# Kernel tuning notes

Hardware: AMD Instinct MI355X
Metric: run time of the kernel (lower is better)

The kernel has to match this reference:

```python
import jax, jax.numpy as jnp
import numpy as np

N, E, FEAT, HID, C, K = 100000, 1600000, 128, 256, 64, 10
AVG_DEG = 16.0

def prelu(x, a):
    return jnp.where(x >= 0, x, a * x)

def setup_inputs() -> dict:
    key = jax.random.key(0)
    ks = jax.random.split(key, 12)
    s = 0.05
    x = jax.random.normal(ks[0], (N, FEAT), jnp.float32)
    edge_index = jax.random.randint(ks[1], (2, E), 0, N, dtype=jnp.int32)
    # GCN-style symmetric norm magnitude ~ 1/deg so K-hop sums stay bounded
    norm = jax.random.uniform(ks[2], (E,), jnp.float32) * (1.0 / AVG_DEG)
    W1 = jax.random.normal(ks[3], (FEAT, HID), jnp.float32) * s
    b1 = jnp.zeros((HID,), jnp.float32)
    W2 = jax.random.normal(ks[4], (HID, HID), jnp.float32) * s
    b2 = jnp.zeros((HID,), jnp.float32)
    W3 = jax.random.normal(ks[5], (HID, HID), jnp.float32) * s
    b3 = jnp.zeros((HID,), jnp.float32)
    W4 = jax.random.normal(ks[6], (HID, C), jnp.float32) * s
    b4 = jnp.zeros((C,), jnp.float32)
    prelu_a = jnp.array(0.25, jnp.float32)
    proj_w = jax.random.normal(ks[7], (C, 1), jnp.float32) * s
    proj_b = jnp.zeros((1,), jnp.float32)
    return {"x": x, "edge_index": edge_index, "norm": norm,
            "W1": W1, "b1": b1, "W2": W2, "b2": b2, "W3": W3, "b3": b3,
            "W4": W4, "b4": b4, "prelu_a": prelu_a,
            "proj_w": proj_w, "proj_b": proj_b}

def reference(x, edge_index, norm, W1, b1, W2, b2, W3, b3, W4, b4, prelu_a, proj_w, proj_b):
    h = prelu(x @ W1 + b1, prelu_a)                      # [N, HID]
    h = prelu((h @ W2 + b2) + h, prelu_a)                # residual Dense
    h = prelu((h @ W3 + b3) + h, prelu_a)                # residual Dense
    z = h @ W4 + b4                                      # [N, C]
    # --- Prop: K hops of norm-weighted scatter-add over edge_index
    src, dst = edge_index[0], edge_index[1]
    def hop(h_cur, _):
        msg = norm[:, None] * h_cur[src]                 # [E, C] gather
        h_nxt = jax.ops.segment_sum(msg, dst, num_segments=N)
        return h_nxt, h_nxt
    _, hs = jax.lax.scan(hop, z, None, length=K)         # [K, N, C]
    pps = jnp.concatenate([z[None], hs], axis=0)         # [K+1, N, C]
    # adaptive per-hop retain score (DAGNN-style)
    score = jax.nn.sigmoid(jnp.einsum('knc,co->kn', pps, proj_w) + proj_b[0])  # [K+1, N]
    out = jnp.einsum('kn,knc->nc', score, pps)           # [N, C]
    return jax.nn.log_softmax(out, axis=1)
```

## Files before the change

kernel.cpp:

```cpp
#include <hip/hip_runtime.h>
#include <stdint.h>
#include <stddef.h>

#define FEATDIM 128
#define HIDDIM  256
#define CDIM    64
#define NHOPS   10

typedef __attribute__((ext_vector_type(8))) short bf16x8;
typedef __attribute__((ext_vector_type(4))) float f32x4;
typedef unsigned short u16;

__device__ __forceinline__ u16 f2bf(float f) {
  uint32_t u = __builtin_bit_cast(uint32_t, f);
  u = (u + 0x7fffu + ((u >> 16) & 1u)) >> 16;
  return (u16)u;
}
__device__ __forceinline__ float bf2f(u16 h) {
  uint32_t u = ((uint32_t)h) << 16;
  return __builtin_bit_cast(float, u);
}
__device__ __forceinline__ float bflo(uint32_t u) {
  return __builtin_bit_cast(float, u << 16);
}
__device__ __forceinline__ float bfhi(uint32_t u) {
  return __builtin_bit_cast(float, u & 0xffff0000u);
}

__device__ __forceinline__ void cvt_one(const float* w, u16* wt, int K, int N, int e) {
  int k = e / N, n = e - k * N;
  wt[(size_t)n * K + k] = f2bf(w[e]);
}
__global__ void k_cvt_w(const float* __restrict__ W1, const float* __restrict__ W2,
                        const float* __restrict__ W3, const float* __restrict__ W4,
                        u16* __restrict__ wt1, u16* __restrict__ wt2,
                        u16* __restrict__ wt3, u16* __restrict__ wt4) {
  const int S1 = FEATDIM * HIDDIM;
  const int S2 = S1 + HIDDIM * HIDDIM;
  const int S3 = S2 + HIDDIM * HIDDIM;
  const int S4 = S3 + HIDDIM * CDIM;
  int e = blockIdx.x * blockDim.x + threadIdx.x;
  if (e < S1)      cvt_one(W1, wt1, FEATDIM, HIDDIM, e);
  else if (e < S2) cvt_one(W2, wt2, HIDDIM, HIDDIM, e - S1);
  else if (e < S3) cvt_one(W3, wt3, HIDDIM, HIDDIM, e - S2);
  else if (e < S4) cvt_one(W4, wt4, HIDDIM, CDIM,  e - S3);
}

template<int K, bool RESID, bool CVT>
__global__ __launch_bounds__(512) void k_gemm_bn(const void* __restrict__ Av, const u16* __restrict__ WT,
                                                 const float* __restrict__ bias, const float* __restrict__ pa_ptr,
                                                 u16* __restrict__ outb, int M) {
  __shared__ alignas(16) u16 Alds[128 * 32];
  __shared__ alignas(16) u16 Blds[256 * 32];
  const int t = threadIdx.x;
  const int w = t >> 6, l = t & 63;
  const int wr = w >> 2, wc = w & 3;
  const int lr = l & 15, lk = l >> 4;
  const int m0 = blockIdx.x * 128;
  const u16* A = (const u16*)Av;
  const float* Af = (const float*)Av;

  f32x4 acc[4][4];
#pragma unroll
  for (int a = 0; a < 4; ++a)
#pragma unroll
    for (int b = 0; b < 4; ++b)
#pragma unroll
      for (int i = 0; i < 4; ++i) acc[a][b][i] = 0.f;

  for (int k0 = 0; k0 < K; k0 += 32) {
    {
      int row = t >> 2, ks = t & 3;
      int gm = m0 + row; if (gm >= M) gm = M - 1;
      bf16x8 v;
      if constexpr (CVT) {
        const float4* p = (const float4*)(Af + (size_t)gm * K + k0 + ks * 8);
        float4 a0 = p[0], a1 = p[1];
        v[0] = (short)f2bf(a0.x); v[1] = (short)f2bf(a0.y);
        v[2] = (short)f2bf(a0.z); v[3] = (short)f2bf(a0.w);
        v[4] = (short)f2bf(a1.x); v[5] = (short)f2bf(a1.y);
        v[6] = (short)f2bf(a1.z); v[7] = (short)f2bf(a1.w);
      } else {
        v = *(const bf16x8*)(A + (size_t)gm * K + k0 + ks * 8);
      }
      int wks = ks ^ ((row >> 1) & 3);
      *(bf16x8*)&Alds[row * 32 + wks * 8] = v;
    }
#pragma unroll
    for (int s = 0; s < 2; ++s) {
      int slot = t + s * 512;
      int row = slot >> 2, ks = slot & 3;
      bf16x8 v = *(const bf16x8*)(WT + (size_t)row * K + k0 + ks * 8);
      int wks = ks ^ ((row >> 1) & 3);
      *(bf16x8*)&Blds[row * 32 + wks * 8] = v;
    }
    __syncthreads();

    bf16x8 fa[4], fb[4];
#pragma unroll
    for (int mr = 0; mr < 4; ++mr) {
      int row = wr * 64 + mr * 16 + lr;
      int ks = lk ^ ((row >> 1) & 3);
      fa[mr] = *(const bf16x8*)&Alds[row * 32 + ks * 8];
    }
#pragma unroll
    for (int nt = 0; nt < 4; ++nt) {
      int r = wc * 64 + nt * 16 + lr;
      int ks = lk ^ ((r >> 1) & 3);
      fb[nt] = *(const bf16x8*)&Blds[r * 32 + ks * 8];
    }
#pragma unroll
    for (int mr = 0; mr < 4; ++mr)
#pragma unroll
      for (int nt = 0; nt < 4; ++nt)
        acc[mr][nt] = __builtin_amdgcn_mfma_f32_16x16x32_bf16(fa[mr], fb[nt], acc[mr][nt], 0, 0, 0);
    __syncthreads();
  }

  const float pa = pa_ptr[0];
#pragma unroll
  for (int mr = 0; mr < 4; ++mr) {
#pragma unroll
    for (int nt = 0; nt < 4; ++nt) {
#pragma unroll
      for (int i = 0; i < 4; ++i) {
        int row = m0 + wr * 64 + mr * 16 + lk * 4 + i;
        int col = wc * 64 + nt * 16 + lr;
        if (row < M) {
          float v = acc[mr][nt][i] + bias[col];
          if constexpr (RESID) v += bf2f(A[(size_t)row * K + col]);
          v = (v >= 0.f) ? v : pa * v;
          outb[(size_t)row * 256 + col] = f2bf(v);
        }
      }
    }
  }
}

__global__ __launch_bounds__(256) void k_gemm_c(const u16* __restrict__ A, const u16* __restrict__ WT,
                                                const float* __restrict__ bias, u16* __restrict__ outb, int M) {
  __shared__ alignas(16) u16 Alds[128 * 32];
  __shared__ alignas(16) u16 Blds[64 * 32];
  const int t = threadIdx.x;
  const int w = t >> 6, l = t & 63;
  const int lr = l & 15, lk = l >> 4;
  const int m0 = blockIdx.x * 128;
  const int K = 256;

  f32x4 acc[2][4];
#pragma unroll
  for (int a = 0; a < 2; ++a)
#pragma unroll
    for (int b = 0; b < 4; ++b)
#pragma unroll
      for (int i = 0; i < 4; ++i) acc[a][b][i] = 0.f;

  for (int k0 = 0; k0 < K; k0 += 32) {
#pragma unroll
    for (int s = 0; s < 2; ++s) {
      int slot = t + s * 256;
      int row = slot >> 2, ks = slot & 3;
      int gm = m0 + row; if (gm >= M) gm = M - 1;
      bf16x8 v = *(const bf16x8*)(A + (size_t)gm * K + k0 + ks * 8);
      int wks = ks ^ ((row >> 1) & 3);
      *(bf16x8*)&Alds[row * 32 + wks * 8] = v;
    }
    {
      int row = t >> 2, ks = t & 3;
      bf16x8 v = *(const bf16x8*)(WT + (size_t)row * K + k0 + ks * 8);
      int wks = ks ^ ((row >> 1) & 3);
      *(bf16x8*)&Blds[row * 32 + wks * 8] = v;
    }
    __syncthreads();

    bf16x8 fa[2], fb[4];
#pragma unroll
    for (int mr = 0; mr < 2; ++mr) {
      int row = w * 32 + mr * 16 + lr;
      int ks = lk ^ ((row >> 1) & 3);
      fa[mr] = *(const bf16x8*)&Alds[row * 32 + ks * 8];
    }
#pragma unroll
    for (int nt = 0; nt < 4; ++nt) {
      int r = nt * 16 + lr;
      int ks = lk ^ ((r >> 1) & 3);
      fb[nt] = *(const bf16x8*)&Blds[r * 32 + ks * 8];
    }
#pragma unroll
    for (int mr = 0; mr < 2; ++mr)
#pragma unroll
      for (int nt = 0; nt < 4; ++nt)
        acc[mr][nt] = __builtin_amdgcn_mfma_f32_16x16x32_bf16(fa[mr], fb[nt], acc[mr][nt], 0, 0, 0);
    __syncthreads();
  }

#pragma unroll
  for (int mr = 0; mr < 2; ++mr) {
#pragma unroll
    for (int nt = 0; nt < 4; ++nt) {
#pragma unroll
      for (int i = 0; i < 4; ++i) {
        int row = m0 + w * 32 + mr * 16 + lk * 4 + i;
        int col = nt * 16 + lr;
        if (row < M) {
          float v = acc[mr][nt][i] + bias[col];
          outb[(size_t)row * CDIM + col] = f2bf(v);
        }
      }
    }
  }
}

__global__ void k_hist(const int* __restrict__ dst, int* __restrict__ cnt, u16* __restrict__ rank, int E) {
  int e = blockIdx.x * blockDim.x + threadIdx.x;
  if (e < E) rank[e] = (u16)atomicAdd(&cnt[dst[e]], 1);
}

__global__ void k_scan1(const int* __restrict__ cnt, int* __restrict__ scn, int* __restrict__ bsum, int n) {
  __shared__ int s[256];
  int i = blockIdx.x * 256 + threadIdx.x;
  int v = (i < n) ? cnt[i] : 0;
  s[threadIdx.x] = v;
  __syncthreads();
  for (int off = 1; off < 256; off <<= 1) {
    int tv = (threadIdx.x >= off) ? s[threadIdx.x - off] : 0;
    __syncthreads();
    s[threadIdx.x] += tv;
    __syncthreads();
  }
  if (i < n) scn[i] = s[threadIdx.x];
  if (threadIdx.x == 255) bsum[blockIdx.x] = s[255];
}

__global__ void k_scan2(int* __restrict__ bsum, int B) {
  __shared__ int s[512];
  int v = (threadIdx.x < B) ? bsum[threadIdx.x] : 0;
  s[threadIdx.x] = v;
  __syncthreads();
  for (int off = 1; off < 512; off <<= 1) {
    int tv = (threadIdx.x >= off) ? s[threadIdx.x - off] : 0;
    __syncthreads();
    s[threadIdx.x] += tv;
    __syncthreads();
  }
  if (threadIdx.x < B) bsum[threadIdx.x] = s[threadIdx.x];
}

__global__ void k_scan3(const int* __restrict__ scn, const int* __restrict__ bsum, int* __restrict__ row_ptr, int n) {
  int i = blockIdx.x * 256 + threadIdx.x;
  if (i < n) {
    int off = (blockIdx.x > 0) ? bsum[blockIdx.x - 1] : 0;
    row_ptr[i + 1] = scn[i] + off;
  }
  if (i == 0) row_ptr[0] = 0;
}

__global__ void k_scatter(const int* __restrict__ src, const int* __restrict__ dst, const float* __restrict__ nrm,
                          const int* __restrict__ row_ptr, const u16* __restrict__ rank,
                          int2* __restrict__ ed, int E) {
  int e = blockIdx.x * blockDim.x + threadIdx.x;
  if (e >= E) return;
  int d = dst[e];
  int pos = row_ptr[d] + (int)rank[e];
  ed[pos] = make_int2(src[e], __builtin_bit_cast(int, nrm[e]));
}

__global__ void k_hop2(const u16* __restrict__ hc, const int* __restrict__ row_ptr,
                       const int2* __restrict__ ed, u16* __restrict__ hn, int N) {
  int n = blockIdx.x * 4 + (threadIdx.x >> 6);
  int l = threadIdx.x & 63;
  int q = l >> 4;
  int cl = l & 15;
  if (n >= N) return;
  int beg = row_ptr[n], end = row_ptr[n + 1];
  int deg = end - beg;

  int2 e0 = make_int2(0, 0);
  int jn = (deg < 64) ? deg : 64;
  if (l < jn) e0 = ed[beg + l];

  const uint2* h64 = (const uint2*)hc;
  float a0 = 0.f, a1 = 0.f, a2 = 0.f, a3 = 0.f;
  for (int j = 0; j < jn; j += 16) {
#pragma unroll
    for (int g = 0; g < 4; ++g) {
      int idx = j + 4 * g + q;
      int s = __shfl(e0.x, idx);
      float w = __builtin_bit_cast(float, __shfl(e0.y, idx));
      uint2 u = h64[(size_t)s * 16 + cl];
      a0 += w * bflo(u.x); a1 += w * bfhi(u.x);
      a2 += w * bflo(u.y); a3 += w * bfhi(u.y);
    }
  }
  for (int i = beg + 64; i < end; i += 4) {
    int ii = i + q;
    bool v = ii < end;
    int2 e = ed[v ? ii : (end - 1)];
    float w = v ? __builtin_bit_cast(float, e.y) : 0.f;
    uint2 u = h64[(size_t)e.x * 16 + cl];
    a0 += w * bflo(u.x); a1 += w * bfhi(u.x);
    a2 += w * bflo(u.y); a3 += w * bfhi(u.y);
  }

  a0 += __shfl_xor(a0, 16); a0 += __shfl_xor(a0, 32);
  a1 += __shfl_xor(a1, 16); a1 += __shfl_xor(a1, 32);
  a2 += __shfl_xor(a2, 16); a2 += __shfl_xor(a2, 32);
  a3 += __shfl_xor(a3, 16); a3 += __shfl_xor(a3, 32);
  if (q == 0) {
    uint2 o;
    o.x = ((uint32_t)f2bf(a1) << 16) | (uint32_t)f2bf(a0);
    o.y = ((uint32_t)f2bf(a3) << 16) | (uint32_t)f2bf(a2);
    ((uint2*)hn)[(size_t)n * 16 + cl] = o;
  }
}

__global__ __launch_bounds__(256) void k_final(const u16* __restrict__ H, const float* __restrict__ pw,
                                               const float* __restrict__ pb, float* __restrict__ out, int N) {
  int n = blockIdx.x * 8 + (threadIdx.x >> 5);
  int cl = threadIdx.x & 31;
  if (n >= N) return;
  const uint32_t* h32 = (const uint32_t*)H;
  float pwx = pw[2 * cl], pwy = pw[2 * cl + 1];
  float pbv = pb[0];
  size_t stride = (size_t)N * 32;

  float vx[NHOPS + 1], vy[NHOPS + 1], p[NHOPS + 1];
#pragma unroll
  for (int k = 0; k <= NHOPS; ++k) {
    uint32_t u = h32[(size_t)k * stride + (size_t)n * 32 + cl];
    vx[k] = bflo(u); vy[k] = bfhi(u);
    p[k] = vx[k] * pwx + vy[k] * pwy;
  }
#pragma unroll
  for (int off = 16; off > 0; off >>= 1) {
#pragma unroll
    for (int k = 0; k <= NHOPS; ++k) p[k] += __shfl_xor(p[k], off);
  }
  float accx = 0.f, accy = 0.f;
#pragma unroll
  for (int k = 0; k <= NHOPS; ++k) {
    float sc = 1.f / (1.f + __expf(-(p[k] + pbv)));
    accx += sc * vx[k];
    accy += sc * vy[k];
  }
  float m = fmaxf(accx, accy);
#pragma unroll
  for (int off = 16; off > 0; off >>= 1) m = fmaxf(m, __shfl_xor(m, off));
  float ex = __expf(accx - m), ey = __expf(accy - m);
  float s = ex + ey;
#pragma unroll
  for (int off = 16; off > 0; off >>= 1) s += __shfl_xor(s, off);
  float ls = __logf(s);
  float2 o = make_float2(accx - m - ls, accy - m - ls);
  *(float2*)&out[(size_t)n * CDIM + 2 * cl] = o;
}

extern "C" void kernel_launch(void* const* d_in, const int* in_sizes, int n_in,
                              void* d_out, int out_size, void* d_ws, size_t ws_size,
                              hipStream_t stream) {
  const float* x   = (const float*)d_in[0];
  const int*   ei  = (const int*)d_in[1];
  const float* nrm = (const float*)d_in[2];
  const float* W1  = (const float*)d_in[3];
  const float* b1  = (const float*)d_in[4];
  const float* W2  = (const float*)d_in[5];
  const float* b2  = (const float*)d_in[6];
  const float* W3  = (const float*)d_in[7];
  const float* b3  = (const float*)d_in[8];
  const float* W4  = (const float*)d_in[9];
  const float* b4  = (const float*)d_in[10];
  const float* pa  = (const float*)d_in[11];
  const float* pw  = (const float*)d_in[12];
  const float* pb  = (const float*)d_in[13];
  float* out = (float*)d_out;

  const int M = in_sizes[0] / FEATDIM;
  const int E = in_sizes[1] / 2;
  const int* srcI = ei;
  const int* dstI = ei + E;

  char* ws = (char*)d_ws;
  const size_t hs = ((size_t)M * CDIM * 2 + 255) & ~(size_t)255;
  size_t o = 11 * hs;
  auto alloc = [&](size_t bytes) { size_t r = o; o += (bytes + 255) & ~(size_t)255; return r; };
  size_t oW1 = alloc((size_t)FEATDIM * HIDDIM * 2);
  size_t oW2 = alloc((size_t)HIDDIM * HIDDIM * 2);
  size_t oW3 = alloc((size_t)HIDDIM * HIDDIM * 2);
  size_t oW4 = alloc((size_t)HIDDIM * CDIM * 2);
  size_t oRP = alloc((size_t)(M + 1) * 4);
  size_t oBS = alloc(4096);
  size_t oED = alloc((size_t)E * 8);

  u16*  H    = (u16*)ws;
  u16*  zb   = H;
  u16*  hA   = (u16*)(ws + 1 * hs);
  u16*  hB   = (u16*)(ws + 5 * hs);
  int*  cnt  = (int*)(ws + 9 * hs);
  int*  scn  = (int*)(ws + 9 * hs + (((size_t)M * 4 + 255) & ~(size_t)255));
  u16*  rank = (u16*)(ws + 9 * hs + 2 * (((size_t)M * 4 + 255) & ~(size_t)255));
  u16*  wt1  = (u16*)(ws + oW1);
  u16*  wt2  = (u16*)(ws + oW2);
  u16*  wt3  = (u16*)(ws + oW3);
  u16*  wt4  = (u16*)(ws + oW4);
  int*  rowp = (int*)(ws + oRP);
  int*  bsum = (int*)(ws + oBS);
  int2* ed   = (int2*)(ws + oED);

  {
    const int tot = FEATDIM * HIDDIM + 2 * HIDDIM * HIDDIM + HIDDIM * CDIM;
    k_cvt_w<<<(tot + 255) / 256, 256, 0, stream>>>(W1, W2, W3, W4, wt1, wt2, wt3, wt4);
  }

  hipMemsetAsync(cnt, 0, (size_t)M * 4, stream);
  k_hist<<<(E + 255) / 256, 256, 0, stream>>>(dstI, cnt, rank, E);
  int nb = (M + 255) / 256;
  k_scan1<<<nb, 256, 0, stream>>>(cnt, scn, bsum, M);
  k_scan2<<<1, 512, 0, stream>>>(bsum, nb);
  k_scan3<<<nb, 256, 0, stream>>>(scn, bsum, rowp, M);
  k_scatter<<<(E + 255) / 256, 256, 0, stream>>>(srcI, dstI, nrm, rowp, rank, ed, E);

  int gB = (M + 127) / 128;
  k_gemm_bn<FEATDIM, false, true ><<<gB, 512, 0, stream>>>(x,  wt1, b1, pa, hA, M);
  k_gemm_bn<HIDDIM,  true,  false><<<gB, 512, 0, stream>>>(hA, wt2, b2, pa, hB, M);
  k_gemm_bn<HIDDIM,  true,  false><<<gB, 512, 0, stream>>>(hB, wt3, b3, pa, hA, M);
  k_gemm_c<<<gB, 256, 0, stream>>>(hA, wt4, b4, zb, M);

  int nblk = (M + 3) / 4;
  size_t hsel = (size_t)M * CDIM;
  for (int k = 0; k < NHOPS; ++k)
    k_hop2<<<nblk, 256, 0, stream>>>(H + (size_t)k * hsel, rowp, ed, H + (size_t)(k + 1) * hsel, M);
  k_final<<<(M + 7) / 8, 256, 0, stream>>>(H, pw, pb, out, M);
}
```

Baseline: 779.8 us.

## Split hop features into 16-channel slabs to shrink gather working set

The propagated feature matrix is stored as four column slabs of 16 bf16 channels each instead of row-major 64 channels. Each hop runs four times, once per slab, with a wave handling 16 edges at a time and 4 lanes per edge. The intent is to make each slab (about 3.2 MB) small enough to stay in cache during random gathers. The cost is four times as many launches and four re-reads of the CSR edge list per hop, with only 32-byte gathers per edge. The GEMM epilogue and the final kernel are updated to use the slab layout.

Measured after the change: 1.533 ms. +96.6%, slower.

```diff
diff --git a/kernel.cpp b/kernel.cpp
--- a/kernel.cpp
+++ b/kernel.cpp
@@ -194,6 +194,7 @@
     __syncthreads();
   }
 
+  const size_t slab = (size_t)M * 16;
 #pragma unroll
   for (int mr = 0; mr < 2; ++mr) {
 #pragma unroll
@@ -204,7 +205,7 @@
         int col = nt * 16 + lr;
         if (row < M) {
           float v = acc[mr][nt][i] + bias[col];
-          outb[(size_t)row * CDIM + col] = f2bf(v);
+          outb[(size_t)nt * slab + (size_t)row * 16 + lr] = f2bf(v);
         }
       }
     }
@@ -265,12 +266,12 @@
   ed[pos] = make_int2(src[e], __builtin_bit_cast(int, nrm[e]));
 }
 
-__global__ void k_hop2(const u16* __restrict__ hc, const int* __restrict__ row_ptr,
-                       const int2* __restrict__ ed, u16* __restrict__ hn, int N) {
+__global__ void k_hop_s(const u16* __restrict__ hcs, const int* __restrict__ row_ptr,
+                        const int2* __restrict__ ed, u16* __restrict__ hns, int N) {
   int n = blockIdx.x * 4 + (threadIdx.x >> 6);
   int l = threadIdx.x & 63;
-  int q = l >> 4;
-  int cl = l & 15;
+  int q = l >> 2;
+  int cl = l & 3;
   if (n >= N) return;
   int beg = row_ptr[n], end = row_ptr[n + 1];
   int deg = end - beg;
@@ -279,38 +280,38 @@
   int jn = (deg < 64) ? deg : 64;
   if (l < jn) e0 = ed[beg + l];
 
-  const uint2* h64 = (const uint2*)hc;
+  const uint2* h8 = (const uint2*)hcs;
   float a0 = 0.f, a1 = 0.f, a2 = 0.f, a3 = 0.f;
   for (int j = 0; j < jn; j += 16) {
-#pragma unroll
-    for (int g = 0; g < 4; ++g) {
-      int idx = j + 4 * g + q;
-      int s = __shfl(e0.x, idx);
-      float w = __builtin_bit_cast(float, __shfl(e0.y, idx));
-      uint2 u = h64[(size_t)s * 16 + cl];
-      a0 += w * bflo(u.x); a1 += w * bfhi(u.x);
-      a2 += w * bflo(u.y); a3 += w * bfhi(u.y);
-    }
-  }
-  for (int i = beg + 64; i < end; i += 4) {
+    int idx = j + q;
+    int s = __shfl(e0.x, idx);
+    float w = __builtin_bit_cast(float, __shfl(e0.y, idx));
+    uint2 u = h8[(size_t)s * 4 + cl];
+    a0 += w * bflo(u.x); a1 += w * bfhi(u.x);
+    a2 += w * bflo(u.y); a3 += w * bfhi(u.y);
+  }
+  for (int i = beg + 64; i < end; i += 16) {
     int ii = i + q;
     bool v = ii < end;
     int2 e = ed[v ? ii : (end - 1)];
     float w = v ? __builtin_bit_cast(float, e.y) : 0.f;
-    uint2 u = h64[(size_t)e.x * 16 + cl];
+    uint2 u = h8[(size_t)e.x * 4 + cl];
     a0 += w * bflo(u.x); a1 += w * bfhi(u.x);
     a2 += w * bflo(u.y); a3 += w * bfhi(u.y);
   }
 
-  a0 += __shfl_xor(a0, 16); a0 += __shfl_xor(a0, 32);
-  a1 += __shfl_xor(a1, 16); a1 += __shfl_xor(a1, 32);
-  a2 += __shfl_xor(a2, 16); a2 += __shfl_xor(a2, 32);
-  a3 += __shfl_xor(a3, 16); a3 += __shfl_xor(a3, 32);
+#pragma unroll
+  for (int off = 4; off < 64; off <<= 1) {
+    a0 += __shfl_xor(a0, off);
+    a1 += __shfl_xor(a1, off);
+    a2 += __shfl_xor(a2, off);
+    a3 += __shfl_xor(a3, off);
+  }
   if (q == 0) {
     uint2 o;
     o.x = ((uint32_t)f2bf(a1) << 16) | (uint32_t)f2bf(a0);
     o.y = ((uint32_t)f2bf(a3) << 16) | (uint32_t)f2bf(a2);
-    ((uint2*)hn)[(size_t)n * 16 + cl] = o;
+    ((uint2*)hns)[(size_t)n * 4 + cl] = o;
   }
 }
 
@@ -322,12 +323,13 @@
   const uint32_t* h32 = (const uint32_t*)H;
   float pwx = pw[2 * cl], pwy = pw[2 * cl + 1];
   float pbv = pb[0];
-  size_t stride = (size_t)N * 32;
+  size_t kstride = (size_t)N * 32;
+  size_t base = (size_t)(cl >> 3) * N * 8 + (size_t)n * 8 + (size_t)(cl & 7);
 
   float vx[NHOPS + 1], vy[NHOPS + 1], p[NHOPS + 1];
 #pragma unroll
   for (int k = 0; k <= NHOPS; ++k) {
-    uint32_t u = h32[(size_t)k * stride + (size_t)n * 32 + cl];
+    uint32_t u = h32[(size_t)k * kstride + base];
     vx[k] = bflo(u); vy[k] = bfhi(u);
     p[k] = vx[k] * pwx + vy[k] * pwy;
   }
@@ -427,7 +429,10 @@
 
   int nblk = (M + 3) / 4;
   size_t hsel = (size_t)M * CDIM;
+  size_t slab = (size_t)M * 16;
   for (int k = 0; k < NHOPS; ++k)
-    k_hop2<<<nblk, 256, 0, stream>>>(H + (size_t)k * hsel, rowp, ed, H + (size_t)(k + 1) * hsel, M);
+    for (int s = 0; s < 4; ++s)
+      k_hop_s<<<nblk, 256, 0, stream>>>(H + (size_t)k * hsel + (size_t)s * slab, rowp, ed,
+                                        H + (size_t)(k + 1) * hsel + (size_t)s * slab, M);
   k_final<<<(M + 7) / 8, 256, 0, stream>>>(H, pw, pb, out, M);
 }
```
